# Kernel optimization log

Measured on AMD Instinct MI355X. Metric: run time of the kernel, lower is better.

Reference implementation:

```python
import jax, jax.numpy as jnp
import numpy as np

N, F, H, T, E, HOR = 50000, 24, 128, 12, 800000, 6


def setup_inputs() -> dict:
    key = jax.random.key(0)
    ks = jax.random.split(key, 16)
    x_seq = jax.random.normal(ks[0], (T, N, F), jnp.float32)
    ei_seq = jax.random.randint(ks[1], (T, 2, E), 0, N, jnp.int32)
    ea_seq = jax.random.uniform(ks[2], (T, E), jnp.float32)
    mask_seq = jax.random.bernoulli(ks[3], 0.9, (T, N))
    s = 1.0 / float(np.sqrt(H))
    def w(k, shape):
        return jax.random.uniform(k, shape, jnp.float32, -s, s)
    params = dict(
        Wz=w(ks[4], (F, H)), Wr=w(ks[5], (F, H)), Wh=w(ks[6], (F, H)),
        bz=jnp.zeros((H,), jnp.float32), br=jnp.zeros((H,), jnp.float32), bh=jnp.zeros((H,), jnp.float32),
        LWz=w(ks[7], (2 * H, H)), LWr=w(ks[8], (2 * H, H)), LWh=w(ks[9], (2 * H, H)),
        Lbz=w(ks[10], (H,)), Lbr=w(ks[11], (H,)), Lbh=w(ks[12], (H,)),
        headW=w(ks[13], (H, F)), headb=w(ks[14], (F,)),
    )
    return dict(x_seq=x_seq, ei_seq=ei_seq, ea_seq=ea_seq, mask_seq=mask_seq, id_seq=0, **params)


def _gcn(x, src, dst, ew, W, b):
    xw = x @ W                                                     # [N,H]
    deg = jnp.zeros((x.shape[0],), xw.dtype).at[dst].add(ew) + 1.0  # in-degree + self-loop
    dinv = jax.lax.rsqrt(deg)
    coef = dinv[src] * ew * dinv[dst]                              # [E]
    agg = jnp.zeros_like(xw).at[dst].add(xw[src] * coef[:, None])
    return agg + xw * (1.0 / deg)[:, None] + b                     # normalized self-loop term


def _cell(x, src, dst, ew, h, p):
    # TGCN (GCN-GRU) cell from pytorch_geometric_temporal
    z = jax.nn.sigmoid(jnp.concatenate([_gcn(x, src, dst, ew, p['Wz'], p['bz']), h], 1) @ p['LWz'] + p['Lbz'])
    r = jax.nn.sigmoid(jnp.concatenate([_gcn(x, src, dst, ew, p['Wr'], p['br']), h], 1) @ p['LWr'] + p['Lbr'])
    htil = jnp.tanh(jnp.concatenate([_gcn(x, src, dst, ew, p['Wh'], p['bh']), h * r], 1) @ p['LWh'] + p['Lbh'])
    return z * h + (1.0 - z) * htil


def _forward(x_seq, ei_seq, ea_seq, mask_seq, p):
    Nn, Hh = x_seq.shape[1], p['LWz'].shape[1]

    # Encoder over T steps: h_store keeps last hidden of every node ever present
    def enc(carry, inp):
        h_store, seen = carry
        x, ei, ew, mask = inp
        h_prev = jnp.where((mask & seen)[:, None], h_store, 0.0)
        h_new = _cell(x, ei[0], ei[1], ew, h_prev, p)
        return (jnp.where(mask[:, None], h_new, h_store), seen | mask), None

    init = (jnp.zeros((Nn, Hh), x_seq.dtype), jnp.zeros((Nn,), bool))
    (h_store, seen), _ = jax.lax.scan(enc, init, (x_seq, ei_seq, ea_seq, mask_seq))

    h_prev = jnp.where((mask_seq[-1] & seen)[:, None], h_store, 0.0)
    src_l, dst_l, ew_l = ei_seq[-1, 0], ei_seq[-1, 1], ea_seq[-1]

    def dec(carry, _):
        h, inp = carry
        h_new = _cell(inp, src_l, dst_l, ew_l, h, p)
        y = h_new @ p['headW'] + p['headb']
        return (h_new, y), y

    _, preds = jax.lax.scan(dec, (h_prev, x_seq[-1]), None, length=HOR)
    return preds  # [horizon, N, out_channels]


def reference(x_seq, ei_seq, ea_seq, mask_seq, id_seq, Wz, Wr, Wh, bz, br, bh,
              LWz, LWr, LWh, Lbz, Lbr, Lbh, headW, headb):
    p = dict(Wz=Wz, Wr=Wr, Wh=Wh, bz=bz, br=br, bh=bh,
             LWz=LWz, LWr=LWr, LWh=LWh, Lbz=Lbz, Lbr=Lbr, Lbh=Lbh,
             headW=headW, headb=headb)
    return _forward(x_seq, ei_seq, ea_seq, mask_seq, p)
```

## Files before the change

kernel.cpp:

```cpp
#include <hip/hip_runtime.h>

#define NN 50000
#define FF 24
#define HH 128
#define TT 12
#define EE 800000
#define HORZ 6


__global__ void k_maskdetect(const unsigned char* __restrict__ m, int* __restrict__ flag) {
    int i = blockIdx.x * 256 + threadIdx.x;
    if (i < 16384 && (i & 3) != 0 && m[i] != 0) atomicOr(flag, 1);
}

__global__ void k_maskconv(const unsigned char* __restrict__ mraw, const int* __restrict__ flag,
                           unsigned char* __restrict__ mout) {
    int i = blockIdx.x * 256 + threadIdx.x;
    if (i >= TT * NN) return;
    if (*flag) mout[i] = (mraw[i] != 0);
    else       mout[i] = (((const int*)mraw)[i] != 0);
}


__global__ void k_hist(const int* __restrict__ ei, int* __restrict__ cnt) {
    int idx = blockIdx.x * 256 + threadIdx.x;
    if (idx >= TT * EE) return;
    int t = idx / EE, e = idx - t * EE;
    int dst = ei[((size_t)t * 2 + 1) * EE + e];
    atomicAdd(&cnt[t * NN + dst], 1);
}

__global__ void k_scan(const int* __restrict__ cnt, int* __restrict__ offs,
                       int* __restrict__ cursor) {
    __shared__ int sums[1024];
    int t = blockIdx.x, tid = threadIdx.x;
    const int per = (NN + 1023) / 1024;
    int base = tid * per;
    int s = 0;
    for (int i = 0; i < per; i++) {
        int idx = base + i;
        if (idx < NN) s += cnt[t * NN + idx];
    }
    sums[tid] = s;
    __syncthreads();
    for (int off = 1; off < 1024; off <<= 1) {
        int tv = (tid >= off) ? sums[tid - off] : 0;
        __syncthreads();
        sums[tid] += tv;
        __syncthreads();
    }
    int run = sums[tid] - s;
    for (int i = 0; i < per; i++) {
        int idx = base + i;
        if (idx < NN) {
            offs[t * (NN + 1) + idx] = run;
            cursor[t * NN + idx] = run;
            run += cnt[t * NN + idx];
        }
    }
    if (tid == 1023) offs[t * (NN + 1) + NN] = sums[1023];
}

__global__ void k_fill(const int* __restrict__ ei, const float* __restrict__ ea,
                       int* __restrict__ cursor, int2* __restrict__ edges) {
    int idx = blockIdx.x * 256 + threadIdx.x;
    if (idx >= TT * EE) return;
    int t = idx / EE, e = idx - t * EE;
    int dst = ei[((size_t)t * 2 + 1) * EE + e];
    int src = ei[((size_t)t * 2 + 0) * EE + e];
    int pos = atomicAdd(&cursor[t * NN + dst], 1);
    edges[(size_t)t * EE + pos] = make_int2(src, __float_as_int(ea[(size_t)t * EE + e]));
}

__global__ void k_degdinv(const int* __restrict__ offs, const int2* __restrict__ edges,
                          float* __restrict__ dinv) {
    int idx = blockIdx.x * 256 + threadIdx.x;
    if (idx >= TT * NN) return;
    int t = idx / NN, n = idx - t * NN;
    int b = offs[t * (NN + 1) + n], en = offs[t * (NN + 1) + n + 1];
    float s = 0.f;
    for (int j = b; j < en; j++) s += __int_as_float(edges[(size_t)t * EE + j].y);
    dinv[idx] = rsqrtf(s + 1.0f);
}

__global__ void k_coef(const int* __restrict__ offs, const float* __restrict__ dinv,
                       int2* __restrict__ edges) {
    int idx = blockIdx.x * 256 + threadIdx.x;
    if (idx >= TT * NN) return;
    int t = idx / NN, n = idx - t * NN;
    int b = offs[t * (NN + 1) + n], en = offs[t * (NN + 1) + n + 1];
    float di = dinv[idx];
    for (int j = b; j < en; j++) {
        int2 p = edges[(size_t)t * EE + j];
        float v = __int_as_float(p.y) * di * dinv[t * NN + p.x];
        edges[(size_t)t * EE + j].y = __float_as_int(v);
    }
}


__global__ void k_fold(const float* __restrict__ Wz, const float* __restrict__ Wr,
                       const float* __restrict__ Wh,
                       const float* __restrict__ bz, const float* __restrict__ br,
                       const float* __restrict__ bh,
                       const float* __restrict__ LWz, const float* __restrict__ LWr,
                       const float* __restrict__ LWh,
                       const float* __restrict__ Lbz, const float* __restrict__ Lbr,
                       const float* __restrict__ Lbh,
                       float* __restrict__ Call, float* __restrict__ b2) {
    int g = blockIdx.x, c = threadIdx.x;
    const float* W  = g == 0 ? Wz : (g == 1 ? Wr : Wh);
    const float* LW = g == 0 ? LWz : (g == 1 ? LWr : LWh);
    const float* bg = g == 0 ? bz : (g == 1 ? br : bh);
    const float* Lb = g == 0 ? Lbz : (g == 1 ? Lbr : Lbh);
    for (int j = 0; j < FF; j++) {
        float a = 0.f;
        for (int k = 0; k < HH; k++) a += W[j * HH + k] * LW[k * HH + c];
        Call[((size_t)g * FF + j) * HH + c] = a;
    }
    float a = Lb[c];
    for (int k = 0; k < HH; k++) a += bg[k] * LW[k * HH + c];
    b2[g * HH + c] = a;
}


__global__ void k_gather(const float* __restrict__ x, const int* __restrict__ offs,
                         const int2* __restrict__ edges,
                         const float* __restrict__ dinv, float* __restrict__ xe) {
    int idx = blockIdx.x * 256 + threadIdx.x;
    if (idx >= NN * FF) return;
    int n = idx / FF, f = idx - n * FF;
    int b = offs[n], en = offs[n + 1];
    float di = dinv[n];
    float acc = x[idx] * di * di;
    for (int j = b; j < en; j++) {
        int2 p = edges[j];
        acc += x[p.x * FF + f] * __int_as_float(p.y);
    }
    xe[idx] = acc;
}


#define FMA8X2(SARR, M0, K)                                                                  \
    {                                                                                        \
        float4 v_;                                                                           \
        v_ = *(const float4*)&SARR[M0 + 0][K];                                               \
        az0 += v_.x*wz0 + v_.y*wz1 + v_.z*wz2 + v_.w*wz3;                                    \
        ar0 += v_.x*wr0 + v_.y*wr1 + v_.z*wr2 + v_.w*wr3;                                    \
        v_ = *(const float4*)&SARR[M0 + 1][K];                                               \
        az1 += v_.x*wz0 + v_.y*wz1 + v_.z*wz2 + v_.w*wz3;                                    \
        ar1 += v_.x*wr0 + v_.y*wr1 + v_.z*wr2 + v_.w*wr3;                                    \
        v_ = *(const float4*)&SARR[M0 + 2][K];                                               \
        az2 += v_.x*wz0 + v_.y*wz1 + v_.z*wz2 + v_.w*wz3;                                    \
        ar2 += v_.x*wr0 + v_.y*wr1 + v_.z*wr2 + v_.w*wr3;                                    \
        v_ = *(const float4*)&SARR[M0 + 3][K];                                               \
        az3 += v_.x*wz0 + v_.y*wz1 + v_.z*wz2 + v_.w*wz3;                                    \
        ar3 += v_.x*wr0 + v_.y*wr1 + v_.z*wr2 + v_.w*wr3;                                    \
        v_ = *(const float4*)&SARR[M0 + 4][K];                                               \
        az4 += v_.x*wz0 + v_.y*wz1 + v_.z*wz2 + v_.w*wz3;                                    \
        ar4 += v_.x*wr0 + v_.y*wr1 + v_.z*wr2 + v_.w*wr3;                                    \
        v_ = *(const float4*)&SARR[M0 + 5][K];                                               \
        az5 += v_.x*wz0 + v_.y*wz1 + v_.z*wz2 + v_.w*wz3;                                    \
        ar5 += v_.x*wr0 + v_.y*wr1 + v_.z*wr2 + v_.w*wr3;                                    \
        v_ = *(const float4*)&SARR[M0 + 6][K];                                               \
        az6 += v_.x*wz0 + v_.y*wz1 + v_.z*wz2 + v_.w*wz3;                                    \
        ar6 += v_.x*wr0 + v_.y*wr1 + v_.z*wr2 + v_.w*wr3;                                    \
        v_ = *(const float4*)&SARR[M0 + 7][K];                                               \
        az7 += v_.x*wz0 + v_.y*wz1 + v_.z*wz2 + v_.w*wz3;                                    \
        ar7 += v_.x*wr0 + v_.y*wr1 + v_.z*wr2 + v_.w*wr3;                                    \
    }

#define FMA8X(SARR, M0, K)                                                        \
    {                                                                             \
        float4 v_;                                                                \
        v_ = *(const float4*)&SARR[M0 + 0][K]; a0 += v_.x*w0 + v_.y*w1 + v_.z*w2 + v_.w*w3; \
        v_ = *(const float4*)&SARR[M0 + 1][K]; a1 += v_.x*w0 + v_.y*w1 + v_.z*w2 + v_.w*w3; \
        v_ = *(const float4*)&SARR[M0 + 2][K]; a2 += v_.x*w0 + v_.y*w1 + v_.z*w2 + v_.w*w3; \
        v_ = *(const float4*)&SARR[M0 + 3][K]; a3 += v_.x*w0 + v_.y*w1 + v_.z*w2 + v_.w*w3; \
        v_ = *(const float4*)&SARR[M0 + 4][K]; a4 += v_.x*w0 + v_.y*w1 + v_.z*w2 + v_.w*w3; \
        v_ = *(const float4*)&SARR[M0 + 5][K]; a5 += v_.x*w0 + v_.y*w1 + v_.z*w2 + v_.w*w3; \
        v_ = *(const float4*)&SARR[M0 + 6][K]; a6 += v_.x*w0 + v_.y*w1 + v_.z*w2 + v_.w*w3; \
        v_ = *(const float4*)&SARR[M0 + 7][K]; a7 += v_.x*w0 + v_.y*w1 + v_.z*w2 + v_.w*w3; \
    }

template <int DOHEAD>
__global__ __launch_bounds__(256) void k_cell(
        const float* __restrict__ xe, const float* __restrict__ hin,
        const unsigned char* __restrict__ gmask,
        const float* __restrict__ Call, const float* __restrict__ b2,
        const float* __restrict__ LWz, const float* __restrict__ LWr,
        const float* __restrict__ LWh,
        const unsigned char* __restrict__ wmask, float* __restrict__ hout,
        const float* __restrict__ headW, const float* __restrict__ headb,
        float* __restrict__ y) {
    __shared__ float s_xe[16][FF];
    __shared__ float s_h0[16][HH];
    __shared__ float s_z[16][HH];
    __shared__ float s_hr[16][HH];
    int nb = blockIdx.x * 16;
    int tid = threadIdx.x;

    for (int i = tid; i < 16 * FF; i += 256) {
        s_xe[i / FF][i % FF] = xe[(size_t)nb * FF + i];
    }
    for (int i = tid; i < 16 * HH; i += 256) {
        int m = i >> 7, k = i & 127;
        float v = hin[((size_t)nb + m) * HH + k];
        if (gmask && !gmask[nb + m]) v = 0.f;
        s_h0[m][k] = v;
    }
    __syncthreads();

    int g = tid >> 7, c = tid & 127;
    int m0 = g * 8;

    {
        const float* Cz   = Call;
        const float* Cr   = Call + (size_t)FF * HH;
        const float* LWzb = LWz + (size_t)HH * HH;
        const float* LWrb = LWr + (size_t)HH * HH;
        float bbz = b2[c], bbr = b2[HH + c];
        float az0 = bbz, az1 = bbz, az2 = bbz, az3 = bbz, az4 = bbz, az5 = bbz, az6 = bbz, az7 = bbz;
        float ar0 = bbr, ar1 = bbr, ar2 = bbr, ar3 = bbr, ar4 = bbr, ar5 = bbr, ar6 = bbr, ar7 = bbr;
#pragma unroll
        for (int k = 0; k < FF; k += 4) {
            float wz0 = Cz[(k + 0) * HH + c], wz1 = Cz[(k + 1) * HH + c];
            float wz2 = Cz[(k + 2) * HH + c], wz3 = Cz[(k + 3) * HH + c];
            float wr0 = Cr[(k + 0) * HH + c], wr1 = Cr[(k + 1) * HH + c];
            float wr2 = Cr[(k + 2) * HH + c], wr3 = Cr[(k + 3) * HH + c];
            FMA8X2(s_xe, m0, k);
        }
#pragma unroll 4
        for (int k = 0; k < HH; k += 4) {
            float wz0 = LWzb[(k + 0) * HH + c], wz1 = LWzb[(k + 1) * HH + c];
            float wz2 = LWzb[(k + 2) * HH + c], wz3 = LWzb[(k + 3) * HH + c];
            float wr0 = LWrb[(k + 0) * HH + c], wr1 = LWrb[(k + 1) * HH + c];
            float wr2 = LWrb[(k + 2) * HH + c], wr3 = LWrb[(k + 3) * HH + c];
            FMA8X2(s_h0, m0, k);
        }
#pragma unroll
        for (int r = 0; r < 8; r++) {
            float az = (r == 0) ? az0 : (r == 1) ? az1 : (r == 2) ? az2 : (r == 3) ? az3
                     : (r == 4) ? az4 : (r == 5) ? az5 : (r == 6) ? az6 : az7;
            float ar = (r == 0) ? ar0 : (r == 1) ? ar1 : (r == 2) ? ar2 : (r == 3) ? ar3
                     : (r == 4) ? ar4 : (r == 5) ? ar5 : (r == 6) ? ar6 : ar7;
            s_z[m0 + r][c]  = 1.f / (1.f + __expf(-az));
            s_hr[m0 + r][c] = (1.f / (1.f + __expf(-ar))) * s_h0[m0 + r][c];
        }
    }
    __syncthreads();

    {
        const float* Ch   = Call + (size_t)2 * FF * HH;
        const float* LWhb = LWh + (size_t)HH * HH;
        float bb = b2[2 * HH + c];
        float a0 = bb, a1 = bb, a2 = bb, a3 = bb, a4 = bb, a5 = bb, a6 = bb, a7 = bb;
#pragma unroll
        for (int k = 0; k < FF; k += 4) {
            float w0 = Ch[(k + 0) * HH + c], w1 = Ch[(k + 1) * HH + c];
            float w2 = Ch[(k + 2) * HH + c], w3 = Ch[(k + 3) * HH + c];
            FMA8X(s_xe, m0, k);
        }
#pragma unroll 4
        for (int k = 0; k < HH; k += 4) {
            float w0 = LWhb[(k + 0) * HH + c], w1 = LWhb[(k + 1) * HH + c];
            float w2 = LWhb[(k + 2) * HH + c], w3 = LWhb[(k + 3) * HH + c];
            FMA8X(s_hr, m0, k);
        }
#pragma unroll
        for (int r = 0; r < 8; r++) {
            float a = (r == 0) ? a0 : (r == 1) ? a1 : (r == 2) ? a2 : (r == 3) ? a3
                    : (r == 4) ? a4 : (r == 5) ? a5 : (r == 6) ? a6 : a7;
            int m = m0 + r;
            float e2 = __expf(2.f * a);
            float ht = 1.f - 2.f / (e2 + 1.f);
            float z = s_z[m][c];
            float h0v = s_h0[m][c];
            float hn = z * h0v + (1.f - z) * ht;
            int n = nb + m;
            if (wmask) {
                if (wmask[n]) hout[(size_t)n * HH + c] = hn;
            } else {
                hout[(size_t)n * HH + c] = hn;
            }
            if (DOHEAD) s_z[m][c] = hn;
        }
    }

    if (DOHEAD) {
        __syncthreads();
        for (int i = tid; i < 16 * FF; i += 256) {
            int m = i / FF, f = i - m * FF;
            float acc = headb[f];
#pragma unroll 8
            for (int cJ = 0; cJ < HH; cJ++) acc += s_z[m][cJ] * headW[cJ * FF + f];
            y[(size_t)nb * FF + i] = acc;
        }
    }
}

extern "C" void kernel_launch(void* const* d_in, const int* in_sizes, int n_in,
                              void* d_out, int out_size, void* d_ws, size_t ws_size,
                              hipStream_t stream) {
    const float* x_seq = (const float*)d_in[0];
    const int*   ei    = (const int*)d_in[1];
    const float* ea    = (const float*)d_in[2];
    const unsigned char* mraw = (const unsigned char*)d_in[3];
    const float* Wz  = (const float*)d_in[5];
    const float* Wr  = (const float*)d_in[6];
    const float* Wh  = (const float*)d_in[7];
    const float* bz  = (const float*)d_in[8];
    const float* br  = (const float*)d_in[9];
    const float* bh  = (const float*)d_in[10];
    const float* LWz = (const float*)d_in[11];
    const float* LWr = (const float*)d_in[12];
    const float* LWh = (const float*)d_in[13];
    const float* Lbz = (const float*)d_in[14];
    const float* Lbr = (const float*)d_in[15];
    const float* Lbh = (const float*)d_in[16];
    const float* headW = (const float*)d_in[17];
    const float* headb = (const float*)d_in[18];
    float* out = (float*)d_out;

    char* wp = (char*)d_ws;
    int*   cnt    = (int*)wp;   wp += sizeof(int) * TT * NN;
    int*   cursor = (int*)wp;   wp += sizeof(int) * TT * NN;
    int*   offs   = (int*)wp;   wp += sizeof(int) * TT * (NN + 1);
    int2*  edges  = (int2*)wp;  wp += sizeof(int2) * (size_t)TT * EE;
    float* dinv   = (float*)wp; wp += sizeof(float) * TT * NN;
    float* hstore = (float*)wp; wp += sizeof(float) * (size_t)NN * HH;
    float* hp     = (float*)wp; wp += sizeof(float) * (size_t)NN * HH;
    float* xebuf  = (float*)wp; wp += sizeof(float) * NN * FF;
    float* Call   = (float*)wp; wp += sizeof(float) * 3 * FF * HH;
    float* b2     = (float*)wp; wp += sizeof(float) * 3 * HH;
    int*   mflag  = (int*)wp;   wp += 256;
    unsigned char* mask = (unsigned char*)wp; wp += TT * NN;
    if (ws_size < (size_t)(wp - (char*)d_ws)) return;

    hipMemsetAsync(mflag, 0, sizeof(int), stream);
    k_maskdetect<<<64, 256, 0, stream>>>(mraw, mflag);
    k_maskconv<<<(TT * NN + 255) / 256, 256, 0, stream>>>(mraw, mflag, mask);

    hipMemsetAsync(cnt, 0, sizeof(int) * TT * NN, stream);
    hipMemsetAsync(hstore, 0, sizeof(float) * NN * HH, stream);
    k_hist<<<(TT * EE + 255) / 256, 256, 0, stream>>>(ei, cnt);
    k_scan<<<TT, 1024, 0, stream>>>(cnt, offs, cursor);
    k_fill<<<(TT * EE + 255) / 256, 256, 0, stream>>>(ei, ea, cursor, edges);
    k_degdinv<<<(TT * NN + 255) / 256, 256, 0, stream>>>(offs, edges, dinv);
    k_coef<<<(TT * NN + 255) / 256, 256, 0, stream>>>(offs, dinv, edges);
    k_fold<<<3, 128, 0, stream>>>(Wz, Wr, Wh, bz, br, bh, LWz, LWr, LWh, Lbz, Lbr, Lbh, Call, b2);

    for (int t = 0; t < TT; t++) {
        const float* xt = x_seq + (size_t)t * NN * FF;
        const unsigned char* mt = mask + (size_t)t * NN;
        k_gather<<<(NN * FF + 255) / 256, 256, 0, stream>>>(
            xt, offs + t * (NN + 1), edges + (size_t)t * EE, dinv + t * NN, xebuf);
        k_cell<0><<<NN / 16, 256, 0, stream>>>(
            xebuf, hstore, mt, Call, b2, LWz, LWr, LWh, mt, hstore,
            nullptr, nullptr, nullptr);
    }

    const int*  offsl  = offs + (TT - 1) * (NN + 1);
    const int2* edgesl = edges + (size_t)(TT - 1) * EE;
    const float* dil   = dinv + (TT - 1) * NN;
    for (int k = 0; k < HORZ; k++) {
        const float* xin = (k == 0) ? (x_seq + (size_t)(TT - 1) * NN * FF)
                                    : (out + (size_t)(k - 1) * NN * FF);
        k_gather<<<(NN * FF + 255) / 256, 256, 0, stream>>>(
            xin, offsl, edgesl, dil, xebuf);
        k_cell<1><<<NN / 16, 256, 0, stream>>>(
            xebuf, (k == 0) ? hstore : hp,
            (k == 0) ? (mask + (size_t)(TT - 1) * NN) : nullptr,
            Call, b2, LWz, LWr, LWh, nullptr, hp,
            headW, headb, out + (size_t)k * NN * FF);
    }
}
```

Baseline: 5.121 ms.

## Vectorize edge gather with float4 and split CSR into SoA with rank-based fill

The gather kernel now has each thread handle four features of a node as a float4 instead of one scalar feature, which cuts repeated edge-list reads per node by a factor of four and widens loads from x. The packed int2 edge array is split into separate source-index and weight arrays. The CSR fill uses the slot index returned by the histogram atomics, so it no longer needs a second pass of atomics on a cursor array. In exchange, an extra rank array of TT*EE ints must be written and read back, and gather parallelism drops to 6 threads per node.

```diff
diff --git a/kernel.cpp b/kernel.cpp
--- a/kernel.cpp
+++ b/kernel.cpp
@@ -22,16 +22,16 @@
 }
 
 
-__global__ void k_hist(const int* __restrict__ ei, int* __restrict__ cnt) {
+__global__ void k_hist(const int* __restrict__ ei, int* __restrict__ cnt,
+                       int* __restrict__ rank) {
     int idx = blockIdx.x * 256 + threadIdx.x;
     if (idx >= TT * EE) return;
     int t = idx / EE, e = idx - t * EE;
     int dst = ei[((size_t)t * 2 + 1) * EE + e];
-    atomicAdd(&cnt[t * NN + dst], 1);
-}
-
-__global__ void k_scan(const int* __restrict__ cnt, int* __restrict__ offs,
-                       int* __restrict__ cursor) {
+    rank[idx] = atomicAdd(&cnt[t * NN + dst], 1);
+}
+
+__global__ void k_scan(const int* __restrict__ cnt, int* __restrict__ offs) {
     __shared__ int sums[1024];
     int t = blockIdx.x, tid = threadIdx.x;
     const int per = (NN + 1023) / 1024;
@@ -54,7 +54,6 @@
         int idx = base + i;
         if (idx < NN) {
             offs[t * (NN + 1) + idx] = run;
-            cursor[t * NN + idx] = run;
             run += cnt[t * NN + idx];
         }
     }
@@ -62,38 +61,39 @@
 }
 
 __global__ void k_fill(const int* __restrict__ ei, const float* __restrict__ ea,
-                       int* __restrict__ cursor, int2* __restrict__ edges) {
+                       const int* __restrict__ offs, const int* __restrict__ rank,
+                       int* __restrict__ srcs, float* __restrict__ eav) {
     int idx = blockIdx.x * 256 + threadIdx.x;
     if (idx >= TT * EE) return;
     int t = idx / EE, e = idx - t * EE;
     int dst = ei[((size_t)t * 2 + 1) * EE + e];
     int src = ei[((size_t)t * 2 + 0) * EE + e];
-    int pos = atomicAdd(&cursor[t * NN + dst], 1);
-    edges[(size_t)t * EE + pos] = make_int2(src, __float_as_int(ea[(size_t)t * EE + e]));
-}
-
-__global__ void k_degdinv(const int* __restrict__ offs, const int2* __restrict__ edges,
+    int pos = offs[t * (NN + 1) + dst] + rank[idx];
+    srcs[(size_t)t * EE + pos] = src;
+    eav[(size_t)t * EE + pos]  = ea[(size_t)t * EE + e];
+}
+
+__global__ void k_degdinv(const int* __restrict__ offs, const float* __restrict__ eav,
                           float* __restrict__ dinv) {
     int idx = blockIdx.x * 256 + threadIdx.x;
     if (idx >= TT * NN) return;
     int t = idx / NN, n = idx - t * NN;
     int b = offs[t * (NN + 1) + n], en = offs[t * (NN + 1) + n + 1];
     float s = 0.f;
-    for (int j = b; j < en; j++) s += __int_as_float(edges[(size_t)t * EE + j].y);
+    for (int j = b; j < en; j++) s += eav[(size_t)t * EE + j];
     dinv[idx] = rsqrtf(s + 1.0f);
 }
 
-__global__ void k_coef(const int* __restrict__ offs, const float* __restrict__ dinv,
-                       int2* __restrict__ edges) {
+__global__ void k_coef(const int* __restrict__ offs, const int* __restrict__ srcs,
+                       const float* __restrict__ dinv, float* __restrict__ eav) {
     int idx = blockIdx.x * 256 + threadIdx.x;
     if (idx >= TT * NN) return;
     int t = idx / NN, n = idx - t * NN;
     int b = offs[t * (NN + 1) + n], en = offs[t * (NN + 1) + n + 1];
     float di = dinv[idx];
     for (int j = b; j < en; j++) {
-        int2 p = edges[(size_t)t * EE + j];
-        float v = __int_as_float(p.y) * di * dinv[t * NN + p.x];
-        edges[(size_t)t * EE + j].y = __float_as_int(v);
+        int s = srcs[(size_t)t * EE + j];
+        eav[(size_t)t * EE + j] *= di * dinv[t * NN + s];
     }
 }
 
@@ -124,19 +124,23 @@
 
 
 __global__ void k_gather(const float* __restrict__ x, const int* __restrict__ offs,
-                         const int2* __restrict__ edges,
+                         const int* __restrict__ srcs, const float* __restrict__ eav,
                          const float* __restrict__ dinv, float* __restrict__ xe) {
     int idx = blockIdx.x * 256 + threadIdx.x;
-    if (idx >= NN * FF) return;
-    int n = idx / FF, f = idx - n * FF;
+    if (idx >= NN * 6) return;
+    int n = idx / 6, q = idx - n * 6;
     int b = offs[n], en = offs[n + 1];
     float di = dinv[n];
-    float acc = x[idx] * di * di;
+    float sc = di * di;
+    float4 acc = *(const float4*)&x[(size_t)n * FF + q * 4];
+    acc.x *= sc; acc.y *= sc; acc.z *= sc; acc.w *= sc;
     for (int j = b; j < en; j++) {
-        int2 p = edges[j];
-        acc += x[p.x * FF + f] * __int_as_float(p.y);
-    }
-    xe[idx] = acc;
+        int s = srcs[j];
+        float w = eav[j];
+        float4 v = *(const float4*)&x[(size_t)s * FF + q * 4];
+        acc.x += v.x * w; acc.y += v.y * w; acc.z += v.z * w; acc.w += v.w * w;
+    }
+    *(float4*)&xe[(size_t)n * FF + q * 4] = acc;
 }
 
 
@@ -323,9 +327,10 @@
 
     char* wp = (char*)d_ws;
     int*   cnt    = (int*)wp;   wp += sizeof(int) * TT * NN;
-    int*   cursor = (int*)wp;   wp += sizeof(int) * TT * NN;
     int*   offs   = (int*)wp;   wp += sizeof(int) * TT * (NN + 1);
-    int2*  edges  = (int2*)wp;  wp += sizeof(int2) * (size_t)TT * EE;
+    int*   rank   = (int*)wp;   wp += sizeof(int) * (size_t)TT * EE;
+    int*   srcs   = (int*)wp;   wp += sizeof(int) * (size_t)TT * EE;
+    float* eav    = (float*)wp; wp += sizeof(float) * (size_t)TT * EE;
     float* dinv   = (float*)wp; wp += sizeof(float) * TT * NN;
     float* hstore = (float*)wp; wp += sizeof(float) * (size_t)NN * HH;
     float* hp     = (float*)wp; wp += sizeof(float) * (size_t)NN * HH;
@@ -342,31 +347,33 @@
 
     hipMemsetAsync(cnt, 0, sizeof(int) * TT * NN, stream);
     hipMemsetAsync(hstore, 0, sizeof(float) * NN * HH, stream);
-    k_hist<<<(TT * EE + 255) / 256, 256, 0, stream>>>(ei, cnt);
-    k_scan<<<TT, 1024, 0, stream>>>(cnt, offs, cursor);
-    k_fill<<<(TT * EE + 255) / 256, 256, 0, stream>>>(ei, ea, cursor, edges);
-    k_degdinv<<<(TT * NN + 255) / 256, 256, 0, stream>>>(offs, edges, dinv);
-    k_coef<<<(TT * NN + 255) / 256, 256, 0, stream>>>(offs, dinv, edges);
+    k_hist<<<(TT * EE + 255) / 256, 256, 0, stream>>>(ei, cnt, rank);
+    k_scan<<<TT, 1024, 0, stream>>>(cnt, offs);
+    k_fill<<<(TT * EE + 255) / 256, 256, 0, stream>>>(ei, ea, offs, rank, srcs, eav);
+    k_degdinv<<<(TT * NN + 255) / 256, 256, 0, stream>>>(offs, eav, dinv);
+    k_coef<<<(TT * NN + 255) / 256, 256, 0, stream>>>(offs, srcs, dinv, eav);
     k_fold<<<3, 128, 0, stream>>>(Wz, Wr, Wh, bz, br, bh, LWz, LWr, LWh, Lbz, Lbr, Lbh, Call, b2);
 
     for (int t = 0; t < TT; t++) {
         const float* xt = x_seq + (size_t)t * NN * FF;
         const unsigned char* mt = mask + (size_t)t * NN;
-        k_gather<<<(NN * FF + 255) / 256, 256, 0, stream>>>(
-            xt, offs + t * (NN + 1), edges + (size_t)t * EE, dinv + t * NN, xebuf);
+        k_gather<<<(NN * 6 + 255) / 256, 256, 0, stream>>>(
+            xt, offs + t * (NN + 1), srcs + (size_t)t * EE, eav + (size_t)t * EE,
+            dinv + t * NN, xebuf);
         k_cell<0><<<NN / 16, 256, 0, stream>>>(
             xebuf, hstore, mt, Call, b2, LWz, LWr, LWh, mt, hstore,
             nullptr, nullptr, nullptr);
     }
 
-    const int*  offsl  = offs + (TT - 1) * (NN + 1);
-    const int2* edgesl = edges + (size_t)(TT - 1) * EE;
+    const int*   offsl = offs + (TT - 1) * (NN + 1);
+    const int*   srcsl = srcs + (size_t)(TT - 1) * EE;
+    const float* eavl  = eav + (size_t)(TT - 1) * EE;
     const float* dil   = dinv + (TT - 1) * NN;
     for (int k = 0; k < HORZ; k++) {
         const float* xin = (k == 0) ? (x_seq + (size_t)(TT - 1) * NN * FF)
                                     : (out + (size_t)(k - 1) * NN * FF);
-        k_gather<<<(NN * FF + 255) / 256, 256, 0, stream>>>(
-            xin, offsl, edgesl, dil, xebuf);
+        k_gather<<<(NN * 6 + 255) / 256, 256, 0, stream>>>(
+            xin, offsl, srcsl, eavl, dil, xebuf);
         k_cell<1><<<NN / 16, 256, 0, stream>>>(
             xebuf, (k == 0) ? hstore : hp,
             (k == 0) ? (mask + (size_t)(TT - 1) * NN) : nullptr,
```

After: 4.472 ms. -12.7%, faster.
